# Kernel tuning notes

Hardware: AMD Instinct MI355X
Metric: run time of the kernel (lower is better)

Reference implementation:

```python
import jax, jax.numpy as jnp
import numpy as np

D_MODEL = 1024
NUM_HEADS = 16
D_K = D_MODEL // NUM_HEADS
SCALE = D_K ** -0.5
NEG = -1e9


def _split_heads(t):
    B, L, D = t.shape
    return t.reshape(B, L, NUM_HEADS, D_K).transpose(0, 2, 1, 3)  # (B,H,L,dk)


def _tropical_scores(Q, K):
    # max over d_k of Q[...,i,d] + K[...,j,d] without materializing (B,H,L,L,dk)
    Qd = jnp.moveaxis(Q, -1, 0)  # (dk,B,H,L)
    Kd = jnp.moveaxis(K, -1, 0)
    B, H, L, _ = Q.shape
    init = jnp.full((B, H, L, L), -jnp.inf, Q.dtype)
    def step(carry, qk):
        q, k = qk  # (B,H,L) each
        return jnp.maximum(carry, q[..., :, None] + k[..., None, :]), None
    out, _ = jax.lax.scan(step, init, (Qd, Kd))
    return out


def setup_inputs() -> dict:
    key = jax.random.key(0)
    ks = jax.random.split(key, 10)
    B, L = 2, 1024
    x = jax.random.normal(ks[0], (B, L, D_MODEL), dtype=jnp.float32)
    # causal mask (B,1,L,L)
    mask = jnp.broadcast_to(jnp.tril(jnp.ones((L, L), dtype=bool)), (B, 1, L, L))
    s = 0.02
    Wq = jax.random.normal(ks[1], (D_MODEL, D_MODEL), jnp.float32) * s
    Wk = jax.random.normal(ks[2], (D_MODEL, D_MODEL), jnp.float32) * s
    Wv = jax.random.normal(ks[3], (D_MODEL, D_MODEL), jnp.float32) * s
    Wo = jax.random.normal(ks[4], (D_MODEL, D_MODEL), jnp.float32) * s
    bq = jnp.zeros((D_MODEL,), jnp.float32)
    bk = jnp.zeros((D_MODEL,), jnp.float32)
    bv = jnp.zeros((D_MODEL,), jnp.float32)
    bo = jnp.zeros((D_MODEL,), jnp.float32)
    # score_gate: weight zero-init, bias = -2.0 (as in torch module)
    Wg = jnp.zeros((NUM_HEADS, D_MODEL), jnp.float32)
    bg = jnp.full((NUM_HEADS,), -2.0, jnp.float32)
    # log temperatures, init_temp=1.0 -> log(1)=0
    log_temps = jnp.zeros((NUM_HEADS,), jnp.float32)
    return {"x": x, "mask": mask, "Wq": Wq, "bq": bq, "Wk": Wk, "bk": bk,
            "Wv": Wv, "bv": bv, "Wo": Wo, "bo": bo, "Wg": Wg, "bg": bg,
            "log_temps": log_temps}


def reference(x, mask, Wq, bq, Wk, bk, Wv, bv, Wo, bo, Wg, bg, log_temps):
    B, L, D = x.shape
    Q = _split_heads(x @ Wq.T + bq)
    K = _split_heads(x @ Wk.T + bk)
    V = _split_heads(x @ Wv.T + bv)
    class_scores = jnp.einsum('bhqd,bhkd->bhqk', Q, K) * SCALE
    trop_scores = _tropical_scores(Q, K) * SCALE
    # per-query, per-head gate g in (0,1): (B,L,H) -> (B,H,L,1)
    g = jax.nn.sigmoid(x @ Wg.T + bg).transpose(0, 2, 1)[..., None]
    scores = g * trop_scores + (1.0 - g) * class_scores
    scores = jnp.where(mask, scores, NEG)
    tau = jnp.clip(jnp.exp(log_temps), 0.02, 10.0).reshape(1, NUM_HEADS, 1, 1)
    attn = jax.nn.softmax(scores / tau, axis=-1)
    out = jnp.einsum('bhqk,bhkd->bhqd', attn, V)
    out = out.transpose(0, 2, 1, 3).reshape(B, L, D)
    return out @ Wo.T + bo, attn
```

## Files before the change

### kernel.cpp

```cpp
#include <hip/hip_runtime.h>


typedef _Float16 f16;
typedef __attribute__((ext_vector_type(2))) _Float16 h2;
typedef __attribute__((ext_vector_type(8))) _Float16 f16x8;
typedef __attribute__((ext_vector_type(4))) float f32x4;

__device__ inline f32x4 mfma_f16(f16x8 a, f16x8 b, f32x4 c) {
    return __builtin_amdgcn_mfma_f32_16x16x32_f16(a, b, c, 0, 0, 0);
}

__device__ inline void async_copy16(const f16* g, f16* l) {
    __builtin_amdgcn_global_load_lds((const __attribute__((address_space(1))) void*)g,
                                     (__attribute__((address_space(3))) void*)l, 16, 0, 0);
}

__global__ __launch_bounds__(256) void cvt_all(const float* __restrict__ x,
                                               const float* __restrict__ Wq,
                                               const float* __restrict__ Wk,
                                               const float* __restrict__ Wv,
                                               const float* __restrict__ Wo,
                                               f16* __restrict__ x16,
                                               f16* __restrict__ w16,
                                               f16* __restrict__ wo16) {
    int i = blockIdx.x * 256 + threadIdx.x;
    const float* s;
    f16* d;
    int off;
    if (i < 524288)       { s = x;  d = x16;             off = i; }
    else if (i < 786432)  { s = Wq; d = w16;             off = i - 524288; }
    else if (i < 1048576) { s = Wk; d = w16 + (1 << 20); off = i - 786432; }
    else if (i < 1310720) { s = Wv; d = w16 + (2 << 20); off = i - 1048576; }
    else                  { s = Wo; d = wo16;            off = i - 1310720; }
    float4 v = *(const float4*)(s + (size_t)off * 4);
    f16 o[4] = {(f16)v.x, (f16)v.y, (f16)v.z, (f16)v.w};
    *(uint2*)(d + (size_t)off * 4) = *(uint2*)o;
}

template <bool OUT16, bool VTR>
__global__ __launch_bounds__(256) void gemm128(const f16* __restrict__ A,
                                               const f16* __restrict__ B,
                                               void* __restrict__ Cv,
                                               const float* __restrict__ b0,
                                               const float* __restrict__ b1,
                                               const float* __restrict__ b2,
                                               f16* __restrict__ vt,
                                               int K, int lda, int ldb, int ldc) {
    __shared__ f16 At[128 * 32];
    __shared__ f16 Bt[64 * 32];
    const int t = threadIdx.x;
    const int m0 = blockIdx.y * 128, n0 = blockIdx.x * 64;
    const int wave = t >> 6, lane = t & 63;
    const int l16 = lane & 15, quad = lane >> 4;
    const int wm = (wave >> 1) * 64, wn = (wave & 1) * 32;
    const int sr = t >> 2, sc = (t & 3) * 8;
    f32x4 acc[4][2] = {};
    for (int k0 = 0; k0 < K; k0 += 32) {
        __syncthreads();
#pragma unroll
        for (int i = 0; i < 2; ++i)
            async_copy16(A + (size_t)(m0 + sr + i * 64) * lda + k0 + sc, &At[t * 8 + i * 2048]);
        async_copy16(B + (size_t)(n0 + sr) * ldb + k0 + sc, &Bt[t * 8]);
        __syncthreads();
        f16x8 af[4], bfr[2];
#pragma unroll
        for (int i = 0; i < 4; ++i)
            af[i] = *(const f16x8*)&At[(wm + i * 16 + l16) * 32 + quad * 8];
#pragma unroll
        for (int i = 0; i < 2; ++i)
            bfr[i] = *(const f16x8*)&Bt[(wn + i * 16 + l16) * 32 + quad * 8];
#pragma unroll
        for (int mi = 0; mi < 4; ++mi)
#pragma unroll
            for (int ni = 0; ni < 2; ++ni)
                acc[mi][ni] = mfma_f16(af[mi], bfr[ni], acc[mi][ni]);
    }
#pragma unroll
    for (int mi = 0; mi < 4; ++mi) {
#pragma unroll
        for (int ni = 0; ni < 2; ++ni) {
            int gcol = n0 + wn + ni * 16 + l16;
            const float* bp = (gcol < 1024) ? b0 : (gcol < 2048 ? b1 : b2);
            float bias = bp[gcol & 1023];
            if (VTR && n0 >= 2048) {
                int hd = gcol - 2048;
                int h = hd >> 6, d = hd & 63;
                int k0r = m0 + wm + mi * 16 + quad * 4;
                int b = k0r >> 10;
                f16 o4[4];
#pragma unroll
                for (int rg = 0; rg < 4; ++rg) o4[rg] = (f16)(acc[mi][ni][rg] + bias);
                *(uint2*)&vt[((size_t)((b * 16 + h) * 64 + d)) * 1024 + (k0r & 1023)] =
                    *(uint2*)o4;
            } else {
#pragma unroll
                for (int rg = 0; rg < 4; ++rg) {
                    int grow = m0 + wm + mi * 16 + quad * 4 + rg;
                    float v = acc[mi][ni][rg] + bias;
                    if (OUT16)
                        ((f16*)Cv)[(size_t)grow * ldc + gcol] = (f16)v;
                    else
                        ((float*)Cv)[(size_t)grow * ldc + gcol] = v;
                }
            }
        }
    }
}

__global__ __launch_bounds__(256) void scores_fused(const f16* __restrict__ qkv16,
                                                    const f16* __restrict__ vt16,
                                                    const float* __restrict__ x,
                                                    const float* __restrict__ Wg,
                                                    const float* __restrict__ bgv,
                                                    const float* __restrict__ log_temps,
                                                    float* __restrict__ attn,
                                                    f16* __restrict__ oh) {
    __shared__ f16 Qs[16][80];
    __shared__ f16 Ssm[16][1032];
    __shared__ float gsm[16];
    const int t = threadIdx.x;
    const int qt = 63 - (blockIdx.x >> 5);
    const int bh = blockIdx.x & 31;
    const int b = bh & 1, h = bh >> 1;
    const int q0 = qt << 4;
    const int lane = t & 63, w = t >> 6;
    const int l16 = lane & 15, quad = lane >> 4;
    const int qmax = q0 + 15;

    {
        int rr = t >> 4, cc = (t & 15) * 4;
        *(uint2*)&Qs[rr][cc] =
            *(const uint2*)(qkv16 + (size_t)(b * 1024 + q0 + rr) * 3072 + h * 64 + cc);
    }
    {
        int row = t >> 4, ch = t & 15;
        const float* xp = x + (size_t)(b * 1024 + q0 + row) * 1024 + ch * 64;
        const float* wp = Wg + (size_t)h * 1024 + ch * 64;
        float acc = 0.f;
#pragma unroll
        for (int j = 0; j < 16; ++j) {
            float4 xv = *(const float4*)(xp + j * 4);
            float4 wv = *(const float4*)(wp + j * 4);
            acc = fmaf(xv.x, wv.x, acc);
            acc = fmaf(xv.y, wv.y, acc);
            acc = fmaf(xv.z, wv.z, acc);
            acc = fmaf(xv.w, wv.w, acc);
        }
#pragma unroll
        for (int o = 8; o > 0; o >>= 1) acc += __shfl_xor(acc, o);
        if (ch == 0) gsm[row] = 1.0f / (1.0f + __expf(-(acc + bgv[h])));
    }
    float tau = __expf(log_temps[h]);
    tau = fminf(fmaxf(tau, 0.02f), 10.0f);
    const float invtau = 1.0f / tau;
    __syncthreads();

    {
        f16x8 qf0 = *(const f16x8*)&Qs[l16][quad * 8];
        f16x8 qf1 = *(const f16x8*)&Qs[l16][32 + quad * 8];
        const f16* Kb = qkv16 + (size_t)(b * 1024 + l16) * 3072 + 1024 + h * 64 + quad * 8;
        for (int kb = w * 16; kb <= qmax; kb += 64) {
            f16x8 kf0 = *(const f16x8*)(Kb + (size_t)kb * 3072);
            f16x8 kf1 = *(const f16x8*)(Kb + (size_t)kb * 3072 + 32);
            f32x4 acc = {};
            acc = mfma_f16(kf0, qf0, acc);
            acc = mfma_f16(kf1, qf1, acc);
            f16 o4[4];
#pragma unroll
            for (int rg = 0; rg < 4; ++rg) o4[rg] = (f16)acc[rg];
            *(uint2*)&Ssm[l16][kb + quad * 4] = *(uint2*)o4;
        }
    }
    __syncthreads();

    {
        const int npass = (qmax >> 9) + 1;
        for (int p = 0; p < npass; ++p) {
            const int k1 = (p << 9) + t;
            const int k2 = k1 + 256;
            const bool a1 = (k1 <= qmax), a2 = (k2 <= qmax);
            if (a1) {
                const f16* Kp1 = qkv16 + (size_t)(b * 1024 + k1) * 3072 + 1024 + h * 64;
                h2 kr1[32], kr2[32];
#pragma unroll
                for (int i = 0; i < 8; ++i) *(f16x8*)&kr1[i * 4] = ((const f16x8*)Kp1)[i];
                if (a2) {
                    const f16* Kp2 = qkv16 + (size_t)(b * 1024 + k2) * 3072 + 1024 + h * 64;
#pragma unroll
                    for (int i = 0; i < 8; ++i) *(f16x8*)&kr2[i * 4] = ((const f16x8*)Kp2)[i];
                }
#pragma unroll 2
                for (int q = 0; q < 16; ++q) {
                    h2 qr[32];
#pragma unroll
                    for (int i = 0; i < 8; ++i)
                        *(f16x8*)&qr[i * 4] = *(const f16x8*)&Qs[q][i * 8];
                    const float g = gsm[q];
                    {
                        float dot = (float)Ssm[q][k1];
                        h2 ta = qr[0] + kr1[0], tb = qr[1] + kr1[1];
#pragma unroll
                        for (int i = 2; i < 32; i += 2) {
                            ta = __builtin_elementwise_max(ta, qr[i] + kr1[i]);
                            tb = __builtin_elementwise_max(tb, qr[i + 1] + kr1[i + 1]);
                        }
                        h2 tc = __builtin_elementwise_max(ta, tb);
                        float tm = fmaxf((float)tc[0], (float)tc[1]);
                        Ssm[q][k1] = (f16)((g * tm + (1.0f - g) * dot) * 0.125f);
                    }
                    if (a2) {
                        float dot = (float)Ssm[q][k2];
                        h2 ta = qr[0] + kr2[0], tb = qr[1] + kr2[1];
#pragma unroll
                        for (int i = 2; i < 32; i += 2) {
                            ta = __builtin_elementwise_max(ta, qr[i] + kr2[i]);
                            tb = __builtin_elementwise_max(tb, qr[i + 1] + kr2[i + 1]);
                        }
                        h2 tc = __builtin_elementwise_max(ta, tb);
                        float tm = fmaxf((float)tc[0], (float)tc[1]);
                        Ssm[q][k2] = (f16)((g * tm + (1.0f - g) * dot) * 0.125f);
                    }
                }
            }
        }
    }
    __syncthreads();

#pragma unroll
    for (int j = 0; j < 4; ++j) {
        int q = w * 4 + j;
        int qg = q0 + q;
        float m = -1e30f;
        for (int k = lane; k <= qg; k += 64) m = fmaxf(m, (float)Ssm[q][k]);
#pragma unroll
        for (int o = 32; o > 0; o >>= 1) m = fmaxf(m, __shfl_xor(m, o));
        float e[16];
        float ssum = 0.f;
#pragma unroll
        for (int i = 0; i < 16; ++i) {
            int k = lane + i * 64;
            if (k <= qg) {
                float v = __expf(((float)Ssm[q][k] - m) * invtau);
                e[i] = v;
                ssum += v;
            } else
                e[i] = 0.f;
        }
#pragma unroll
        for (int o = 32; o > 0; o >>= 1) ssum += __shfl_xor(ssum, o);
        float inv = 1.0f / ssum;
        float* orow = attn + ((size_t)((b * 16 + h) * 1024 + qg) << 10);
#pragma unroll
        for (int i = 0; i < 16; ++i) {
            int k = lane + i * 64;
            float val = e[i] * inv;
            orow[k] = val;
            Ssm[q][k] = (f16)val;
        }
    }
    __syncthreads();

    {
        const int dw = w * 16;
        f32x4 acc = {};
        const int nkt = (q0 + 47) >> 5;
        const f16* Vb = vt16 + ((size_t)((b * 16 + h) * 64 + dw + l16)) * 1024 + quad * 8;
#pragma unroll 4
        for (int kt = 0; kt < nkt; ++kt) {
            const int kb = kt << 5;
            f16x8 a = *(const f16x8*)&Ssm[l16][kb + quad * 8];
            f16x8 bf = *(const f16x8*)(Vb + kb);
            acc = mfma_f16(a, bf, acc);
        }
#pragma unroll
        for (int rg = 0; rg < 4; ++rg)
            oh[(size_t)(b * 1024 + q0 + quad * 4 + rg) * 1024 + h * 64 + dw + l16] =
                (f16)acc[rg];
    }
}

extern "C" void kernel_launch(void* const* d_in, const int* in_sizes, int n_in,
                              void* d_out, int out_size, void* d_ws, size_t ws_size,
                              hipStream_t stream) {
    const float* x  = (const float*)d_in[0];
    const float* Wq = (const float*)d_in[2];
    const float* bq = (const float*)d_in[3];
    const float* Wk = (const float*)d_in[4];
    const float* bk = (const float*)d_in[5];
    const float* Wv = (const float*)d_in[6];
    const float* bv = (const float*)d_in[7];
    const float* Wo = (const float*)d_in[8];
    const float* bo = (const float*)d_in[9];
    const float* Wg = (const float*)d_in[10];
    const float* bg = (const float*)d_in[11];
    const float* lt = (const float*)d_in[12];
    float* out = (float*)d_out;
    float* attn = out + (size_t)2 * 1024 * 1024;

    char* ws = (char*)d_ws;
    const size_t MB = (size_t)1 << 20;
    f16*   x16   = (f16*)ws;
    f16*   w16   = (f16*)(ws + 4 * MB);
    f16*   wo16  = (f16*)(ws + 10 * MB);
    f16*   qkv16 = (f16*)(ws + 12 * MB);
    f16*   vt16  = (f16*)(ws + 24 * MB);
    f16*   oh16  = (f16*)(ws + 29 * MB);

    cvt_all<<<6144, 256, 0, stream>>>(x, Wq, Wk, Wv, Wo, x16, w16, wo16);
    gemm128<true, true><<<dim3(48, 16), 256, 0, stream>>>(x16, w16, qkv16, bq, bk, bv,
                                                          vt16, 1024, 1024, 1024, 3072);
    scores_fused<<<2048, 256, 0, stream>>>(qkv16, vt16, x, Wg, bg, lt, attn, oh16);
    gemm128<false, false><<<dim3(16, 16), 256, 0, stream>>>(oh16, wo16, out, bo, bo, bo,
                                                            nullptr, 1024, 1024, 1024, 1024);
}
```

Before: 320.6 us.

## Halve query tile to 8 rows and hoist gate projection into separate kernel

The scores kernel now processes 8 query rows per block instead of 16, doubling the grid to 4096 blocks and adding a launch bound requesting 7 blocks per SM. The sigmoid gate projection is moved out into a new gate_kernel that writes a per-row, per-head buffer, which the scores kernel reads. The aim is better load balance across the causal triangle and higher occupancy. In exchange, each K row is reused across fewer queries in the tropical loop, and half of each MFMA's output is discarded.

Result: slower. 466.2 us (+45.4%).

```diff
diff --git a/kernel.cpp b/kernel.cpp
--- a/kernel.cpp
+++ b/kernel.cpp
@@ -37,6 +37,31 @@
     *(uint2*)(d + (size_t)off * 4) = *(uint2*)o;
 }
 
+__global__ __launch_bounds__(256) void gate_kernel(const float* __restrict__ x,
+                                                   const float* __restrict__ Wg,
+                                                   const float* __restrict__ bg,
+                                                   float* __restrict__ gbuf) {
+    const int row = blockIdx.x;
+    const int t = threadIdx.x;
+    const int h = t >> 4, li = t & 15;
+    const float* xp = x + (size_t)row * 1024;
+    const float* wp = Wg + (size_t)h * 1024;
+    float acc = 0.f;
+#pragma unroll
+    for (int j = 0; j < 16; ++j) {
+        int d = li * 4 + j * 64;
+        float4 xv = *(const float4*)(xp + d);
+        float4 wv = *(const float4*)(wp + d);
+        acc = fmaf(xv.x, wv.x, acc);
+        acc = fmaf(xv.y, wv.y, acc);
+        acc = fmaf(xv.z, wv.z, acc);
+        acc = fmaf(xv.w, wv.w, acc);
+    }
+#pragma unroll
+    for (int o = 8; o > 0; o >>= 1) acc += __shfl_xor(acc, o);
+    if (li == 0) gbuf[(size_t)row * 16 + h] = 1.0f / (1.0f + __expf(-(acc + bg[h])));
+}
+
 template <bool OUT16, bool VTR>
 __global__ __launch_bounds__(256) void gemm128(const f16* __restrict__ A,
                                                const f16* __restrict__ B,
@@ -107,57 +132,38 @@
     }
 }
 
-__global__ __launch_bounds__(256) void scores_fused(const f16* __restrict__ qkv16,
-                                                    const f16* __restrict__ vt16,
-                                                    const float* __restrict__ x,
-                                                    const float* __restrict__ Wg,
-                                                    const float* __restrict__ bgv,
-                                                    const float* __restrict__ log_temps,
-                                                    float* __restrict__ attn,
-                                                    f16* __restrict__ oh) {
-    __shared__ f16 Qs[16][80];
-    __shared__ f16 Ssm[16][1032];
-    __shared__ float gsm[16];
+__global__ __launch_bounds__(256, 7) void scores_fused(const f16* __restrict__ qkv16,
+                                                       const f16* __restrict__ vt16,
+                                                       const float* __restrict__ gbuf,
+                                                       const float* __restrict__ log_temps,
+                                                       float* __restrict__ attn,
+                                                       f16* __restrict__ oh) {
+    __shared__ f16 Qs[8][80];
+    __shared__ f16 Ssm[8][1032];
+    __shared__ float gsm[8];
     const int t = threadIdx.x;
-    const int qt = 63 - (blockIdx.x >> 5);
+    const int qt = 127 - (blockIdx.x >> 5);
     const int bh = blockIdx.x & 31;
     const int b = bh & 1, h = bh >> 1;
-    const int q0 = qt << 4;
+    const int q0 = qt << 3;
     const int lane = t & 63, w = t >> 6;
     const int l16 = lane & 15, quad = lane >> 4;
-    const int qmax = q0 + 15;
-
-    {
+    const int qmax = q0 + 7;
+
+    if (t < 128) {
         int rr = t >> 4, cc = (t & 15) * 4;
         *(uint2*)&Qs[rr][cc] =
             *(const uint2*)(qkv16 + (size_t)(b * 1024 + q0 + rr) * 3072 + h * 64 + cc);
     }
-    {
-        int row = t >> 4, ch = t & 15;
-        const float* xp = x + (size_t)(b * 1024 + q0 + row) * 1024 + ch * 64;
-        const float* wp = Wg + (size_t)h * 1024 + ch * 64;
-        float acc = 0.f;
-#pragma unroll
-        for (int j = 0; j < 16; ++j) {
-            float4 xv = *(const float4*)(xp + j * 4);
-            float4 wv = *(const float4*)(wp + j * 4);
-            acc = fmaf(xv.x, wv.x, acc);
-            acc = fmaf(xv.y, wv.y, acc);
-            acc = fmaf(xv.z, wv.z, acc);
-            acc = fmaf(xv.w, wv.w, acc);
-        }
-#pragma unroll
-        for (int o = 8; o > 0; o >>= 1) acc += __shfl_xor(acc, o);
-        if (ch == 0) gsm[row] = 1.0f / (1.0f + __expf(-(acc + bgv[h])));
-    }
+    if (t < 8) gsm[t] = gbuf[(size_t)(b * 1024 + q0 + t) * 16 + h];
     float tau = __expf(log_temps[h]);
     tau = fminf(fmaxf(tau, 0.02f), 10.0f);
     const float invtau = 1.0f / tau;
     __syncthreads();
 
     {
-        f16x8 qf0 = *(const f16x8*)&Qs[l16][quad * 8];
-        f16x8 qf1 = *(const f16x8*)&Qs[l16][32 + quad * 8];
+        f16x8 qf0 = *(const f16x8*)&Qs[l16 & 7][quad * 8];
+        f16x8 qf1 = *(const f16x8*)&Qs[l16 & 7][32 + quad * 8];
         const f16* Kb = qkv16 + (size_t)(b * 1024 + l16) * 3072 + 1024 + h * 64 + quad * 8;
         for (int kb = w * 16; kb <= qmax; kb += 64) {
             f16x8 kf0 = *(const f16x8*)(Kb + (size_t)kb * 3072);
@@ -165,10 +171,12 @@
             f32x4 acc = {};
             acc = mfma_f16(kf0, qf0, acc);
             acc = mfma_f16(kf1, qf1, acc);
-            f16 o4[4];
-#pragma unroll
-            for (int rg = 0; rg < 4; ++rg) o4[rg] = (f16)acc[rg];
-            *(uint2*)&Ssm[l16][kb + quad * 4] = *(uint2*)o4;
+            if (l16 < 8) {
+                f16 o4[4];
+#pragma unroll
+                for (int rg = 0; rg < 4; ++rg) o4[rg] = (f16)acc[rg];
+                *(uint2*)&Ssm[l16][kb + quad * 4] = *(uint2*)o4;
+            }
         }
     }
     __syncthreads();
@@ -190,7 +198,7 @@
                     for (int i = 0; i < 8; ++i) *(f16x8*)&kr2[i * 4] = ((const f16x8*)Kp2)[i];
                 }
 #pragma unroll 2
-                for (int q = 0; q < 16; ++q) {
+                for (int q = 0; q < 8; ++q) {
                     h2 qr[32];
 #pragma unroll
                     for (int i = 0; i < 8; ++i)
@@ -227,8 +235,8 @@
     __syncthreads();
 
 #pragma unroll
-    for (int j = 0; j < 4; ++j) {
-        int q = w * 4 + j;
+    for (int j = 0; j < 2; ++j) {
+        int q = w * 2 + j;
         int qg = q0 + q;
         float m = -1e30f;
         for (int k = lane; k <= qg; k += 64) m = fmaxf(m, (float)Ssm[q][k]);
@@ -263,19 +271,21 @@
     {
         const int dw = w * 16;
         f32x4 acc = {};
-        const int nkt = (q0 + 47) >> 5;
+        const int nkt = (q0 + 39) >> 5;
         const f16* Vb = vt16 + ((size_t)((b * 16 + h) * 64 + dw + l16)) * 1024 + quad * 8;
 #pragma unroll 4
         for (int kt = 0; kt < nkt; ++kt) {
             const int kb = kt << 5;
-            f16x8 a = *(const f16x8*)&Ssm[l16][kb + quad * 8];
+            f16x8 a = *(const f16x8*)&Ssm[l16 & 7][kb + quad * 8];
             f16x8 bf = *(const f16x8*)(Vb + kb);
             acc = mfma_f16(a, bf, acc);
         }
-#pragma unroll
-        for (int rg = 0; rg < 4; ++rg)
-            oh[(size_t)(b * 1024 + q0 + quad * 4 + rg) * 1024 + h * 64 + dw + l16] =
-                (f16)acc[rg];
+        if (quad < 2) {
+#pragma unroll
+            for (int rg = 0; rg < 4; ++rg)
+                oh[(size_t)(b * 1024 + q0 + quad * 4 + rg) * 1024 + h * 64 + dw + l16] =
+                    (f16)acc[rg];
+        }
     }
 }
 
@@ -304,12 +314,14 @@
     f16*   wo16  = (f16*)(ws + 10 * MB);
     f16*   qkv16 = (f16*)(ws + 12 * MB);
     f16*   vt16  = (f16*)(ws + 24 * MB);
+    float* gbuf  = (float*)(ws + 28 * MB);
     f16*   oh16  = (f16*)(ws + 29 * MB);
 
     cvt_all<<<6144, 256, 0, stream>>>(x, Wq, Wk, Wv, Wo, x16, w16, wo16);
+    gate_kernel<<<2048, 256, 0, stream>>>(x, Wg, bg, gbuf);
     gemm128<true, true><<<dim3(48, 16), 256, 0, stream>>>(x16, w16, qkv16, bq, bk, bv,
                                                           vt16, 1024, 1024, 1024, 3072);
-    scores_fused<<<2048, 256, 0, stream>>>(qkv16, vt16, x, Wg, bg, lt, attn, oh16);
+    scores_fused<<<4096, 256, 0, stream>>>(qkv16, vt16, gbuf, lt, attn, oh16);
     gemm128<false, false><<<dim3(16, 16), 256, 0, stream>>>(oh16, wo16, out, bo, bo, bo,
                                                             nullptr, 1024, 1024, 1024, 1024);
 }
```
